# Performance work log

Hardware: AMD Instinct MI355X
Metric: run time of the kernel (lower is better)

The kernel has to match this reference:

```python
import jax, jax.numpy as jnp
import numpy as np

N_NODES = 100000
N_EDGES = 1600000
IN_DIM = 160
HID = 128
BN_EPS = 1e-5


def setup_inputs() -> dict:
    key = jax.random.key(0)
    ks = jax.random.split(key, 16)
    d = {}
    d['x'] = jax.random.normal(ks[0], (N_NODES, IN_DIM), dtype=jnp.float32)
    d['edge_index'] = jax.random.randint(ks[1], (2, N_EDGES), 0, N_NODES, dtype=jnp.int64)
    dims = [(IN_DIM, HID), (HID, HID), (HID, HID)]
    for i, (fi, fo) in enumerate(dims):
        s = 1.0 / np.sqrt(fi)
        d[f'wl{i}'] = jax.random.normal(ks[2 + 4 * i], (fi, fo), dtype=jnp.float32) * s
        d[f'wr{i}'] = jax.random.normal(ks[3 + 4 * i], (fi, fo), dtype=jnp.float32) * s
        d[f'bl{i}'] = jnp.zeros((fo,), dtype=jnp.float32)
        d[f'g{i}'] = jnp.ones((fo,), dtype=jnp.float32)
        d[f'be{i}'] = jnp.zeros((fo,), dtype=jnp.float32)
        d[f'rm{i}'] = jax.random.normal(ks[4 + 4 * i], (fo,), dtype=jnp.float32) * 0.1
        d[f'rv{i}'] = jnp.ones((fo,), dtype=jnp.float32)
    d['lin_w'] = jax.random.normal(ks[14], (HID, 1), dtype=jnp.float32) * (1.0 / np.sqrt(HID))
    d['lin_b'] = jnp.zeros((1,), dtype=jnp.float32)
    return d


def _sage_bn_relu(h, src, dst, wl, wr, bl, g, be, rm, rv):
    # mean neighbor aggregation: gather messages at src, scatter-mean to dst
    msg = h[src]                                            # [E, d]
    agg = jax.ops.segment_sum(msg, dst, num_segments=N_NODES)
    cnt = jax.ops.segment_sum(jnp.ones((msg.shape[0],), h.dtype), dst, num_segments=N_NODES)
    mean = agg / jnp.maximum(cnt, 1.0)[:, None]             # nodes w/o in-edges -> 0
    out = mean @ wl + bl + h @ wr                           # SAGEConv (root_weight=True)
    # BatchNorm1d (inference: running stats) + ReLU
    out = (out - rm) * (g * jax.lax.rsqrt(rv + BN_EPS)) + be
    return jax.nn.relu(out)


def reference(x, edge_index,
              wl0, wr0, bl0, g0, be0, rm0, rv0,
              wl1, wr1, bl1, g1, be1, rm1, rv1,
              wl2, wr2, bl2, g2, be2, rm2, rv2,
              lin_w, lin_b):
    src, dst = edge_index[0], edge_index[1]
    h = _sage_bn_relu(x, src, dst, wl0, wr0, bl0, g0, be0, rm0, rv0)
    h = _sage_bn_relu(h, src, dst, wl1, wr1, bl1, g1, be1, rm1, rv1)
    h = _sage_bn_relu(h, src, dst, wl2, wr2, bl2, g2, be2, rm2, rv2)
    return (h @ lin_w + lin_b)[:, 0]                        # [N]
```

## Files before the change

### kernel.cpp

```cpp
#include <hip/hip_runtime.h>

#define N_NODES 100000
#define N_EDGES 1600000
#define IN_DIM 160
#define HID 128
#define BN_EPS 1e-5f

#define M_PAD 100096
#define NBUCK 196
#define BSH 9
#define EPB 8192
#define NHB (NBUCK * NBUCK)
#define NSB 38
#define LPAD 132

typedef unsigned int uint;
typedef unsigned short ushort;
typedef __attribute__((ext_vector_type(8))) short bf16x8;
typedef __attribute__((ext_vector_type(4))) float f32x4;
typedef __attribute__((ext_vector_type(2))) float f32x2;

__device__ __forceinline__ ushort bf16rn(float f) {
    uint u = __float_as_uint(f);
    u += 0x7fffu + ((u >> 16) & 1u);
    return (ushort)(u >> 16);
}
__device__ __forceinline__ float bflo(uint u) { return __uint_as_float(u << 16); }
__device__ __forceinline__ float bfhi(uint u) { return __uint_as_float(u & 0xffff0000u); }


__device__ __forceinline__ void prep_body(int ob, int lane, const float* __restrict__ wl,
                                          const float* __restrict__ wr,
                                          ushort* __restrict__ Bf, int K) {
    int kb = ob >> 4;
    int tt = ob & 15;
    int n = tt * 16 + (lane & 15);
    int k0 = kb * 32 + (lane >> 4) * 8;
    ushort* dst = Bf + ((size_t)(kb * 16 + tt) * 64 + lane) * 8;
#pragma unroll
    for (int e = 0; e < 8; ++e) {
        int k = k0 + e;
        float v = (n < HID) ? wl[k * HID + n] : wr[k * HID + (n - HID)];
        dst[e] = bf16rn(v);
    }
}

#define PREP0_B 20
#define PREP1_B 16
#define INIT_GRID (NBUCK + PREP0_B + 2 * PREP1_B + 2)

__global__ __launch_bounds__(256) void init_kernel(
    const int* __restrict__ dst, int* __restrict__ ghist,
    const float* __restrict__ wl0, const float* __restrict__ wr0,
    const float* __restrict__ wl1, const float* __restrict__ wr1,
    const float* __restrict__ wl2, const float* __restrict__ wr2,
    ushort* __restrict__ Bf0, ushort* __restrict__ Bf1, ushort* __restrict__ Bf2,
    const float* __restrict__ bl0, const float* __restrict__ g0,
    const float* __restrict__ be0, const float* __restrict__ rm0,
    const float* __restrict__ rv0,
    const float* __restrict__ bl1, const float* __restrict__ g1,
    const float* __restrict__ be1, const float* __restrict__ rm1,
    const float* __restrict__ rv1,
    const float* __restrict__ bl2, const float* __restrict__ g2,
    const float* __restrict__ be2, const float* __restrict__ rm2,
    const float* __restrict__ rv2,
    float* __restrict__ bnscale, float* __restrict__ bnshift) {
    __shared__ int hist[NBUCK];
    int b = blockIdx.x, t = threadIdx.x;
    if (b < NBUCK) {
        for (int i = t; i < NBUCK; i += 256) hist[i] = 0;
        __syncthreads();
        int e0 = b * EPB;
        for (int i = 0; i < EPB; i += 256) {
            int e = e0 + i + t;
            if (e < N_EDGES) atomicAdd(&hist[dst[e] >> BSH], 1);
        }
        __syncthreads();
        for (int i = t; i < NBUCK; i += 256) ghist[i * NBUCK + b] = hist[i];
    } else if (b < NBUCK + PREP0_B) {
        int ob = (b - NBUCK) * 4 + (t >> 6);
        prep_body(ob, t & 63, wl0, wr0, Bf0, IN_DIM);
    } else if (b < NBUCK + PREP0_B + PREP1_B) {
        int ob = (b - NBUCK - PREP0_B) * 4 + (t >> 6);
        prep_body(ob, t & 63, wl1, wr1, Bf1, HID);
    } else if (b < NBUCK + PREP0_B + 2 * PREP1_B) {
        int ob = (b - NBUCK - PREP0_B - PREP1_B) * 4 + (t >> 6);
        prep_body(ob, t & 63, wl2, wr2, Bf2, HID);
    } else {
        int tt = (b - (NBUCK + PREP0_B + 2 * PREP1_B)) * 256 + t;
        if (tt < 3 * HID) {
            int L = tt >> 7, j = tt & 127;
            const float* bl = (L == 0) ? bl0 : (L == 1) ? bl1 : bl2;
            const float* gg = (L == 0) ? g0  : (L == 1) ? g1  : g2;
            const float* be = (L == 0) ? be0 : (L == 1) ? be1 : be2;
            const float* rm = (L == 0) ? rm0 : (L == 1) ? rm1 : rm2;
            const float* rv = (L == 0) ? rv0 : (L == 1) ? rv1 : rv2;
            float s = gg[j] * rsqrtf(rv[j] + BN_EPS);
            bnscale[tt] = s;
            bnshift[tt] = (bl[j] - rm[j]) * s + be[j];
        }
    }
}


__global__ __launch_bounds__(256) void scan1_kernel(const int* __restrict__ ghist,
                                                    int* __restrict__ bsum) {
    __shared__ int wsum[4];
    int b = blockIdx.x, t = threadIdx.x;
    int i4 = b * 256 + t;
    int4 v = (i4 * 4 < NHB) ? ((const int4*)ghist)[i4] : make_int4(0, 0, 0, 0);
    int s = v.x + v.y + v.z + v.w;
#pragma unroll
    for (int off = 32; off; off >>= 1) s += __shfl_down(s, off);
    if ((t & 63) == 0) wsum[t >> 6] = s;
    __syncthreads();
    if (t == 0) bsum[b] = wsum[0] + wsum[1] + wsum[2] + wsum[3];
}

__global__ void scan2_kernel(const int* __restrict__ bsum, int* __restrict__ boff,
                             int* __restrict__ gbb) {
    int lane = threadIdx.x;
    int v = (lane < NSB) ? bsum[lane] : 0;
    int s = v;
#pragma unroll
    for (int off = 1; off <= 32; off <<= 1) {
        int t2 = __shfl_up(s, off);
        if (lane >= off) s += t2;
    }
    if (lane < NSB) boff[lane] = s - v;
    if (lane == 0) gbb[NBUCK] = N_EDGES;
}

__global__ __launch_bounds__(256) void scan3_kernel(int* __restrict__ ghist,
                                                    const int* __restrict__ boff,
                                                    int* __restrict__ gbb) {
    __shared__ int ts[256];
    int b = blockIdx.x, t = threadIdx.x;
    int i4 = b * 256 + t;
    bool ok = (i4 * 4) < NHB;
    int4 v = ok ? ((const int4*)ghist)[i4] : make_int4(0, 0, 0, 0);
    int s = v.x + v.y + v.z + v.w;
    ts[t] = s;
    __syncthreads();
    for (int off = 1; off < 256; off <<= 1) {
        int a = (t >= off) ? ts[t - off] : 0;
        __syncthreads();
        ts[t] += a;
        __syncthreads();
    }
    int excl = boff[b] + ((t > 0) ? ts[t - 1] : 0);
    if (ok) {
        int idx = i4 * 4;
        int4 w;
        w.x = excl;
        w.y = excl + v.x;
        w.z = excl + v.x + v.y;
        w.w = excl + v.x + v.y + v.z;
        ((int4*)ghist)[i4] = w;
        if (idx % NBUCK == 0) gbb[idx / NBUCK] = w.x;
    }
}


__global__ __launch_bounds__(256) void bucket_csr_kernel(const uint* __restrict__ scat,
                                                         const int* __restrict__ gbb,
                                                         int* __restrict__ prow,
                                                         int* __restrict__ deg,
                                                         int* __restrict__ peidx) {
    __shared__ int cnt[512], fl[512], pref[512];
    __shared__ int ts[256];
    __shared__ int tot_s;
    int b = blockIdx.x, t = threadIdx.x;
    int beg = gbb[b], end = gbb[b + 1];
    int pb = beg + b * 8192;
    cnt[t] = 0; cnt[t + 256] = 0;
    __syncthreads();
    for (int i = beg + t; i < end; i += 256)
        atomicAdd(&cnt[scat[i] >> 17], 1);
    __syncthreads();
    int c0 = cnt[2 * t], c1 = cnt[2 * t + 1];
    int p0 = (c0 + 15) & ~15, p1 = (c1 + 15) & ~15;
    ts[t] = p0 + p1;
    __syncthreads();
    for (int off = 1; off < 256; off <<= 1) {
        int v = (t >= off) ? ts[t - off] : 0;
        __syncthreads();
        ts[t] += v;
        __syncthreads();
    }
    int ex = (t > 0) ? ts[t - 1] : 0;
    pref[2 * t] = ex;
    pref[2 * t + 1] = ex + p0;
    fl[t] = 0; fl[t + 256] = 0;
    if (t == 255) tot_s = ts[255];
    int g0 = b * 512 + 2 * t;
    if (g0 < N_NODES) { prow[g0] = pb + ex; deg[g0] = c0; }
    if (g0 + 1 < N_NODES) { prow[g0 + 1] = pb + ex + p0; deg[g0 + 1] = c1; }
    __syncthreads();
    int tot = tot_s;
    for (int i = t; i < tot; i += 256) peidx[pb + i] = N_NODES;
    __syncthreads();
    for (int i = beg + t; i < end; i += 256) {
        uint w = scat[i];
        int nl = (int)(w >> 17);
        int lp = atomicAdd(&fl[nl], 1);
        peidx[pb + pref[nl] + lp] = (int)(w & 0x1FFFFu);
    }
}

template <int K, bool AFP32>
__device__ __forceinline__ void gemm_body(int bx, int t, ushort* ldsA,
                                          const void* __restrict__ A_,
                                          const ushort* __restrict__ Bf,
                                          ushort* __restrict__ tl,
                                          ushort* __restrict__ troot) {
    constexpr int CPR = K / 8;
    constexpr int FULLG = CPR & ~7;
    const int m0b = bx * 64;

#pragma unroll
    for (int i = 0; i < (64 * CPR) / 256; ++i) {
        int cidx = i * 256 + t;
        int row = cidx / CPR;
        int j = cidx - row * CPR;
        bf16x8 v;
        if (AFP32) {
            const float* A = (const float*)A_;
            int m = m0b + row;
            float4 f0 = make_float4(0.f, 0.f, 0.f, 0.f), f1 = f0;
            if (m < N_NODES) {
                f0 = *(const float4*)(A + (size_t)m * K + j * 8);
                f1 = *(const float4*)(A + (size_t)m * K + j * 8 + 4);
            }
            v[0] = (short)bf16rn(f0.x); v[1] = (short)bf16rn(f0.y);
            v[2] = (short)bf16rn(f0.z); v[3] = (short)bf16rn(f0.w);
            v[4] = (short)bf16rn(f1.x); v[5] = (short)bf16rn(f1.y);
            v[6] = (short)bf16rn(f1.z); v[7] = (short)bf16rn(f1.w);
        } else {
            const ushort* A = (const ushort*)A_;
            v = *(const bf16x8*)(A + (size_t)(m0b + row) * K + j * 8);
        }
        int swz = (j < FULLG) ? ((j & ~7) | ((j ^ row) & 7))
                              : ((j & ~3) | ((j ^ row) & 3));
        *(bf16x8*)&ldsA[row * K + swz * 8] = v;
    }
    __syncthreads();

    const int lane = t & 63;
    const int wv = t >> 6;
    const int col = lane & 15;
    const int q = lane >> 4;
    const int rh = wv & 1;
    const int ch = wv >> 1;
    const int row0 = rh * 32 + col;
    f32x4 acc0[8], acc1[8];
#pragma unroll
    for (int tt = 0; tt < 8; ++tt) {
        acc0[tt] = (f32x4){0.f, 0.f, 0.f, 0.f};
        acc1[tt] = (f32x4){0.f, 0.f, 0.f, 0.f};
    }

#pragma unroll
    for (int kb = 0; kb < K / 32; ++kb) {
        int jj = kb * 4 + q;
        int swzj = (jj < FULLG) ? ((jj & ~7) | ((jj ^ col) & 7))
                                : ((jj & ~3) | ((jj ^ col) & 3));
        bf16x8 a0 = *(const bf16x8*)&ldsA[row0 * K + swzj * 8];
        bf16x8 a1 = *(const bf16x8*)&ldsA[(row0 + 16) * K + swzj * 8];
        const ushort* bp = Bf + ((size_t)((kb * 16 + ch * 8) * 64) + lane) * 8;
#pragma unroll
        for (int tt = 0; tt < 8; ++tt) {
            bf16x8 bfr = *(const bf16x8*)(bp + (size_t)tt * 64 * 8);
            acc0[tt] = __builtin_amdgcn_mfma_f32_16x16x32_bf16(a0, bfr, acc0[tt], 0, 0, 0);
            acc1[tt] = __builtin_amdgcn_mfma_f32_16x16x32_bf16(a1, bfr, acc1[tt], 0, 0, 0);
        }
    }

    __syncthreads();
    ushort(*rp)[16][LPAD] = (ushort(*)[16][LPAD])ldsA;
    ushort* outp = ch ? troot : tl;
#pragma unroll
    for (int mt = 0; mt < 2; ++mt) {
        const f32x4* ac = mt ? acc1 : acc0;
#pragma unroll
        for (int tt = 0; tt < 8; ++tt)
#pragma unroll
            for (int r = 0; r < 4; ++r)
                rp[wv][q * 4 + r][tt * 16 + col] = bf16rn(ac[tt][r]);
        int mbase = m0b + rh * 32 + mt * 16;
#pragma unroll
        for (int i = 0; i < 4; ++i) {
            int lin = i * 64 + lane;
            int row = lin >> 4;
            int c16 = lin & 15;
            bf16x8 v = *(const bf16x8*)&rp[wv][row][c16 * 8];
            *(bf16x8*)(outp + (size_t)(mbase + row) * HID + c16 * 8) = v;
        }
    }
}

__global__ __launch_bounds__(256) void scatter_gemm1_kernel(
    const int* __restrict__ src, const int* __restrict__ dst,
    const int* __restrict__ ghist, uint* __restrict__ scat,
    const float* __restrict__ x, const ushort* __restrict__ Bf0,
    ushort* __restrict__ tl, ushort* __restrict__ troot) {
    constexpr int LDSE = (64 * IN_DIM > 4 * 16 * LPAD) ? 64 * IN_DIM : 4 * 16 * LPAD;
    __shared__ ushort ldsA[LDSE];
    int b = blockIdx.x, t = threadIdx.x;
    if (b < NBUCK) {
        int* base = (int*)ldsA;
        int* fill = base + NBUCK;
        for (int i = t; i < NBUCK; i += 256) { base[i] = ghist[i * NBUCK + b]; fill[i] = 0; }
        __syncthreads();
        int e0 = b * EPB;
        for (int i = 0; i < EPB; i += 256) {
            int e = e0 + i + t;
            if (e < N_EDGES) {
                int d = dst[e];
                int sv = src[e];
                int bk = d >> BSH;
                int lp = atomicAdd(&fill[bk], 1);
                scat[base[bk] + lp] = (uint)sv | ((uint)(d & 511) << 17);
            }
        }
    } else {
        gemm_body<IN_DIM, true>(b - NBUCK, t, ldsA, x, Bf0, tl, troot);
    }
}

__global__ __launch_bounds__(256) void fused_agg_gemm_kernel(
    const ushort* __restrict__ tl_in, const ushort* __restrict__ troot_in,
    const int* __restrict__ prow, const int* __restrict__ deg_,
    const int* __restrict__ peidx,
    const float* __restrict__ bnscale, const float* __restrict__ bnshift,
    const ushort* __restrict__ Bf,
    ushort* __restrict__ tl_out, ushort* __restrict__ troot_out) {
    constexpr int K = HID;
    constexpr int LDSE = (64 * K > 4 * 16 * LPAD) ? 64 * K : 4 * 16 * LPAD;
    __shared__ ushort ldsA[LDSE];
    const int t = threadIdx.x;
    const int lane = t & 63;
    const int wv = t >> 6;
    const int m0b = blockIdx.x * 64;
    const int g = lane >> 4;
    const int s = lane & 15;
    const int gsel = (lane & 48) << 2;

    for (int r = 0; r < 4; ++r) {
        const int row = wv * 16 + r * 4 + g;
        const int n = m0b + row;
        const bool valid = (n < N_NODES);
        const int nn = valid ? n : 0;
        int pbeg = prow[nn];
        int dg = valid ? deg_[nn] : 0;
        int myb = (dg + 15) >> 4;

        f32x2 acc2[4];
#pragma unroll
        for (int i = 0; i < 4; ++i) acc2[i] = (f32x2){0.f, 0.f};

        bool act = (0 < myb);
        int idx = act ? peidx[pbeg + s] : N_NODES;
        int b = 0;
        while (__any(act)) {
            uint4 u[16];
#pragma unroll
            for (int jj = 0; jj < 16; ++jj) {
                int srcj = __builtin_amdgcn_ds_bpermute(gsel | (jj << 2), idx);
                u[jj] = *(const uint4*)(tl_in + (size_t)srcj * HID + s * 8);
            }
            ++b;
            bool actn = (b < myb);
            int idxn = actn ? peidx[pbeg + b * 16 + s] : N_NODES;
#pragma unroll
            for (int jj = 0; jj < 16; ++jj) {
                acc2[0] += (f32x2){bflo(u[jj].x), bfhi(u[jj].x)};
                acc2[1] += (f32x2){bflo(u[jj].y), bfhi(u[jj].y)};
                acc2[2] += (f32x2){bflo(u[jj].z), bfhi(u[jj].z)};
                acc2[3] += (f32x2){bflo(u[jj].w), bfhi(u[jj].w)};
            }
            act = actn; idx = idxn;
        }

        float inv = 1.0f / (float)((dg > 0) ? dg : 1);
        uint4 rv = *(const uint4*)(troot_in + (size_t)nn * HID + s * 8);
        float4 sc0 = *(const float4*)(bnscale + s * 8);
        float4 sc1 = *(const float4*)(bnscale + s * 8 + 4);
        float4 sh0 = *(const float4*)(bnshift + s * 8);
        float4 sh1 = *(const float4*)(bnshift + s * 8 + 4);
        float vm = valid ? 1.0f : 0.0f;
        float o[8];
        o[0] = fmaxf(fmaf(fmaf(acc2[0].x, inv, bflo(rv.x)), sc0.x, sh0.x), 0.f) * vm;
        o[1] = fmaxf(fmaf(fmaf(acc2[0].y, inv, bfhi(rv.x)), sc0.y, sh0.y), 0.f) * vm;
        o[2] = fmaxf(fmaf(fmaf(acc2[1].x, inv, bflo(rv.y)), sc0.z, sh0.z), 0.f) * vm;
        o[3] = fmaxf(fmaf(fmaf(acc2[1].y, inv, bfhi(rv.y)), sc0.w, sh0.w), 0.f) * vm;
        o[4] = fmaxf(fmaf(fmaf(acc2[2].x, inv, bflo(rv.z)), sc1.x, sh1.x), 0.f) * vm;
        o[5] = fmaxf(fmaf(fmaf(acc2[2].y, inv, bfhi(rv.z)), sc1.y, sh1.y), 0.f) * vm;
        o[6] = fmaxf(fmaf(fmaf(acc2[3].x, inv, bflo(rv.w)), sc1.z, sh1.z), 0.f) * vm;
        o[7] = fmaxf(fmaf(fmaf(acc2[3].y, inv, bfhi(rv.w)), sc1.w, sh1.w), 0.f) * vm;

        bf16x8 pk;
#pragma unroll
        for (int e = 0; e < 8; ++e) pk[e] = (short)bf16rn(o[e]);
        int swz = (s & ~7) | ((s ^ row) & 7);
        *(bf16x8*)&ldsA[row * K + swz * 8] = pk;
    }
    __syncthreads();

    const int col = lane & 15;
    const int q = lane >> 4;
    const int rh = wv & 1;
    const int ch = wv >> 1;
    const int row0 = rh * 32 + col;
    f32x4 acc0[8], acc1[8];
#pragma unroll
    for (int tt = 0; tt < 8; ++tt) {
        acc0[tt] = (f32x4){0.f, 0.f, 0.f, 0.f};
        acc1[tt] = (f32x4){0.f, 0.f, 0.f, 0.f};
    }
#pragma unroll
    for (int kb = 0; kb < K / 32; ++kb) {
        int jj = kb * 4 + q;
        int swzj = (jj & ~7) | ((jj ^ col) & 7);
        bf16x8 a0 = *(const bf16x8*)&ldsA[row0 * K + swzj * 8];
        bf16x8 a1 = *(const bf16x8*)&ldsA[(row0 + 16) * K + swzj * 8];
        const ushort* bp = Bf + ((size_t)((kb * 16 + ch * 8) * 64) + lane) * 8;
#pragma unroll
        for (int tt = 0; tt < 8; ++tt) {
            bf16x8 bfr = *(const bf16x8*)(bp + (size_t)tt * 64 * 8);
            acc0[tt] = __builtin_amdgcn_mfma_f32_16x16x32_bf16(a0, bfr, acc0[tt], 0, 0, 0);
            acc1[tt] = __builtin_amdgcn_mfma_f32_16x16x32_bf16(a1, bfr, acc1[tt], 0, 0, 0);
        }
    }

    __syncthreads();
    ushort(*rp)[16][LPAD] = (ushort(*)[16][LPAD])ldsA;
    ushort* outp = ch ? troot_out : tl_out;
#pragma unroll
    for (int mt = 0; mt < 2; ++mt) {
        const f32x4* ac = mt ? acc1 : acc0;
#pragma unroll
        for (int tt = 0; tt < 8; ++tt)
#pragma unroll
            for (int rr = 0; rr < 4; ++rr)
                rp[wv][q * 4 + rr][tt * 16 + col] = bf16rn(ac[tt][rr]);
        int mbase = m0b + rh * 32 + mt * 16;
#pragma unroll
        for (int i = 0; i < 4; ++i) {
            int lin = i * 64 + lane;
            int rowi = lin >> 4;
            int c16 = lin & 15;
            bf16x8 v = *(const bf16x8*)&rp[wv][rowi][c16 * 8];
            *(bf16x8*)(outp + (size_t)(mbase + rowi) * HID + c16 * 8) = v;
        }
    }
}

__global__ __launch_bounds__(256) void agg_final_kernel(
    const ushort* __restrict__ tl_, const ushort* __restrict__ troot_,
    const int* __restrict__ prow, const int* __restrict__ deg_,
    const int* __restrict__ peidx,
    const float* __restrict__ bnscale, const float* __restrict__ bnshift,
    const float* __restrict__ linw, const float* __restrict__ linb,
    float* __restrict__ out) {
    const int lane = threadIdx.x & 63;
    const int wvg = (blockIdx.x * 256 + (int)threadIdx.x) >> 6;
    const int g = lane >> 4;
    const int s = lane & 15;
    const int n = wvg * 4 + g;

    int pbeg = prow[n];
    int dg = deg_[n];
    int myb = (dg + 15) >> 4;

    f32x2 acc2[4];
#pragma unroll
    for (int i = 0; i < 4; ++i) acc2[i] = (f32x2){0.f, 0.f};

    const int gsel = (lane & 48) << 2;

    bool act = (0 < myb);
    int idx = act ? peidx[pbeg + s] : N_NODES;
    int b = 0;
    while (__any(act)) {
        uint4 u[16];
#pragma unroll
        for (int jj = 0; jj < 16; ++jj) {
            int srcj = __builtin_amdgcn_ds_bpermute(gsel | (jj << 2), idx);
            u[jj] = *(const uint4*)(tl_ + (size_t)srcj * HID + s * 8);
        }
        ++b;
        bool actn = (b < myb);
        int idxn = actn ? peidx[pbeg + b * 16 + s] : N_NODES;
#pragma unroll
        for (int jj = 0; jj < 16; ++jj) {
            acc2[0] += (f32x2){bflo(u[jj].x), bfhi(u[jj].x)};
            acc2[1] += (f32x2){bflo(u[jj].y), bfhi(u[jj].y)};
            acc2[2] += (f32x2){bflo(u[jj].z), bfhi(u[jj].z)};
            acc2[3] += (f32x2){bflo(u[jj].w), bfhi(u[jj].w)};
        }
        act = actn; idx = idxn;
    }

    float inv = 1.0f / (float)((dg > 0) ? dg : 1);
    uint4 rv = *(const uint4*)(troot_ + (size_t)n * HID + s * 8);
    float4 sc0 = *(const float4*)(bnscale + s * 8);
    float4 sc1 = *(const float4*)(bnscale + s * 8 + 4);
    float4 sh0 = *(const float4*)(bnshift + s * 8);
    float4 sh1 = *(const float4*)(bnshift + s * 8 + 4);
    float o[8];
    o[0] = fmaxf(fmaf(fmaf(acc2[0].x, inv, bflo(rv.x)), sc0.x, sh0.x), 0.f);
    o[1] = fmaxf(fmaf(fmaf(acc2[0].y, inv, bfhi(rv.x)), sc0.y, sh0.y), 0.f);
    o[2] = fmaxf(fmaf(fmaf(acc2[1].x, inv, bflo(rv.y)), sc0.z, sh0.z), 0.f);
    o[3] = fmaxf(fmaf(fmaf(acc2[1].y, inv, bfhi(rv.y)), sc0.w, sh0.w), 0.f);
    o[4] = fmaxf(fmaf(fmaf(acc2[2].x, inv, bflo(rv.z)), sc1.x, sh1.x), 0.f);
    o[5] = fmaxf(fmaf(fmaf(acc2[2].y, inv, bfhi(rv.z)), sc1.y, sh1.y), 0.f);
    o[6] = fmaxf(fmaf(fmaf(acc2[3].x, inv, bflo(rv.w)), sc1.z, sh1.z), 0.f);
    o[7] = fmaxf(fmaf(fmaf(acc2[3].y, inv, bfhi(rv.w)), sc1.w, sh1.w), 0.f);

    float4 w0 = *(const float4*)(linw + s * 8);
    float4 w1 = *(const float4*)(linw + s * 8 + 4);
    float p = o[0] * w0.x + o[1] * w0.y + o[2] * w0.z + o[3] * w0.w +
              o[4] * w1.x + o[5] * w1.y + o[6] * w1.z + o[7] * w1.w;
#pragma unroll
    for (int off = 1; off < 16; off <<= 1) p += __shfl_xor(p, off);
    if (s == 0) out[n] = p + linb[0];
}


extern "C" void kernel_launch(void* const* d_in, const int* in_sizes, int n_in,
                              void* d_out, int out_size, void* d_ws, size_t ws_size,
                              hipStream_t stream) {
    const float* x    = (const float*)d_in[0];
    const int*   ei   = (const int*)d_in[1];
    const int*   esrc = ei;
    const int*   edst = ei + N_EDGES;
    const float* wl[3]; const float* wr[3]; const float* bl[3];
    const float* g[3];  const float* be[3]; const float* rm[3]; const float* rv[3];
    for (int i = 0; i < 3; ++i) {
        wl[i] = (const float*)d_in[2 + 7 * i];
        wr[i] = (const float*)d_in[3 + 7 * i];
        bl[i] = (const float*)d_in[4 + 7 * i];
        g[i]  = (const float*)d_in[5 + 7 * i];
        be[i] = (const float*)d_in[6 + 7 * i];
        rm[i] = (const float*)d_in[7 + 7 * i];
        rv[i] = (const float*)d_in[8 + 7 * i];
    }
    const float* lin_w = (const float*)d_in[23];
    const float* lin_b = (const float*)d_in[24];
    float* out = (float*)d_out;

    char* ws = (char*)d_ws;
    size_t off = 0;
    auto carve = [&](size_t bytes) -> void* {
        void* p = ws + off;
        off += (bytes + 255) & ~(size_t)255;
        return p;
    };
    int*    prow   = (int*)carve((size_t)(N_NODES + 8) * sizeof(int));
    int*    deg    = (int*)carve((size_t)(N_NODES + 8) * sizeof(int));
    int*    peidx  = (int*)carve((size_t)3210000 * sizeof(int));
    uint*   scat   = (uint*)carve((size_t)N_EDGES * sizeof(uint));
    int*    ghist  = (int*)carve((size_t)(NSB * 1024) * sizeof(int));
    int*    gbb    = (int*)carve((NBUCK + 4) * sizeof(int));
    int*    bsum   = (int*)carve((NSB + 2) * sizeof(int));
    int*    boff   = (int*)carve((NSB + 2) * sizeof(int));
    ushort* tl0    = (ushort*)carve((size_t)(M_PAD + 1) * HID * sizeof(ushort));
    ushort* troot0 = (ushort*)carve((size_t)M_PAD * HID * sizeof(ushort));
    ushort* tl1    = (ushort*)carve((size_t)(M_PAD + 1) * HID * sizeof(ushort));
    ushort* troot1 = (ushort*)carve((size_t)M_PAD * HID * sizeof(ushort));
    ushort* Bf0    = (ushort*)carve(256 * IN_DIM * sizeof(ushort));
    ushort* Bf1    = (ushort*)carve(256 * HID * sizeof(ushort));
    ushort* Bf2    = (ushort*)carve(256 * HID * sizeof(ushort));
    float*  bnsc   = (float*)carve(3 * HID * sizeof(float));
    float*  bnsh   = (float*)carve(3 * HID * sizeof(float));
    (void)ws_size; (void)n_in; (void)in_sizes; (void)out_size;

    const int GEMM_GRID = M_PAD / 64;
    const int AGGF_GRID = N_NODES / 16;

    init_kernel<<<INIT_GRID, 256, 0, stream>>>(
        edst, ghist,
        wl[0], wr[0], wl[1], wr[1], wl[2], wr[2], Bf0, Bf1, Bf2,
        bl[0], g[0], be[0], rm[0], rv[0],
        bl[1], g[1], be[1], rm[1], rv[1],
        bl[2], g[2], be[2], rm[2], rv[2],
        bnsc, bnsh);
    scan1_kernel<<<NSB, 256, 0, stream>>>(ghist, bsum);
    scan2_kernel<<<1, 64, 0, stream>>>(bsum, boff, gbb);
    scan3_kernel<<<NSB, 256, 0, stream>>>(ghist, boff, gbb);
    scatter_gemm1_kernel<<<NBUCK + GEMM_GRID, 256, 0, stream>>>(
        esrc, edst, ghist, scat, x, Bf0, tl0, troot0);
    bucket_csr_kernel<<<NBUCK, 256, 0, stream>>>(scat, gbb, prow, deg, peidx);

    fused_agg_gemm_kernel<<<GEMM_GRID, 256, 0, stream>>>(
        tl0, troot0, prow, deg, peidx, bnsc, bnsh, Bf1, tl1, troot1);
    fused_agg_gemm_kernel<<<GEMM_GRID, 256, 0, stream>>>(
        tl1, troot1, prow, deg, peidx, bnsc + HID, bnsh + HID, Bf2, tl0, troot0);
    agg_final_kernel<<<AGGF_GRID, 256, 0, stream>>>(
        tl0, troot0, prow, deg, peidx, bnsc + 2 * HID, bnsh + 2 * HID,
        lin_w, lin_b, out);
}
```

Before: 435.1 us.

## Merge preprocessing kernels into one cooperative kernel with grid syncs

Replaces the init, three scan, scatter and bucket-CSR kernel launches with a single cooperative kernel that separates phases with grid-wide syncs. The layer-0 GEMM is split out into its own kernel instead of sharing a launch with the edge scatter. BN scale/shift loads are hoisted out of the per-row loop in the fused aggregation kernel. The aim is to cut launch overhead and gaps between tiny kernels, at the cost of losing the scatter/GEMM overlap and adding grid-sync latency.

Result: slower. 634.0 us (+45.7%).

```diff
diff --git a/kernel.cpp b/kernel.cpp
--- a/kernel.cpp
+++ b/kernel.cpp
@@ -1,4 +1,5 @@
 #include <hip/hip_runtime.h>
+#include <hip/hip_cooperative_groups.h>
 
 #define N_NODES 100000
 #define N_EDGES 1600000
@@ -20,6 +21,8 @@
 typedef __attribute__((ext_vector_type(4))) float f32x4;
 typedef __attribute__((ext_vector_type(2))) float f32x2;
 
+namespace cg = cooperative_groups;
+
 __device__ __forceinline__ ushort bf16rn(float f) {
     uint u = __float_as_uint(f);
     u += 0x7fffu + ((u >> 16) & 1u);
@@ -27,7 +30,6 @@
 }
 __device__ __forceinline__ float bflo(uint u) { return __uint_as_float(u << 16); }
 __device__ __forceinline__ float bfhi(uint u) { return __uint_as_float(u & 0xffff0000u); }
-
 
 __device__ __forceinline__ void prep_body(int ob, int lane, const float* __restrict__ wl,
                                           const float* __restrict__ wr,
@@ -47,164 +49,172 @@
 
 #define PREP0_B 20
 #define PREP1_B 16
-#define INIT_GRID (NBUCK + PREP0_B + 2 * PREP1_B + 2)
-
-__global__ __launch_bounds__(256) void init_kernel(
-    const int* __restrict__ dst, int* __restrict__ ghist,
-    const float* __restrict__ wl0, const float* __restrict__ wr0,
-    const float* __restrict__ wl1, const float* __restrict__ wr1,
-    const float* __restrict__ wl2, const float* __restrict__ wr2,
-    ushort* __restrict__ Bf0, ushort* __restrict__ Bf1, ushort* __restrict__ Bf2,
-    const float* __restrict__ bl0, const float* __restrict__ g0,
-    const float* __restrict__ be0, const float* __restrict__ rm0,
-    const float* __restrict__ rv0,
-    const float* __restrict__ bl1, const float* __restrict__ g1,
-    const float* __restrict__ be1, const float* __restrict__ rm1,
-    const float* __restrict__ rv1,
-    const float* __restrict__ bl2, const float* __restrict__ g2,
-    const float* __restrict__ be2, const float* __restrict__ rm2,
-    const float* __restrict__ rv2,
-    float* __restrict__ bnscale, float* __restrict__ bnshift) {
-    __shared__ int hist[NBUCK];
-    int b = blockIdx.x, t = threadIdx.x;
+#define COOP_GRID (NBUCK + PREP0_B + 2 * PREP1_B + 2)
+
+struct PreArgs {
+    const int* edst; const int* esrc;
+    int* ghist; uint* scat; int* gbb; int* bsum; int* boff;
+    int* prow; int* deg; int* peidx;
+    const float *wl0, *wr0, *wl1, *wr1, *wl2, *wr2;
+    ushort *Bf0, *Bf1, *Bf2;
+    const float *bl0, *g0, *be0, *rm0, *rv0;
+    const float *bl1, *g1, *be1, *rm1, *rv1;
+    const float *bl2, *g2, *be2, *rm2, *rv2;
+    float *bnsc, *bnsh;
+};
+
+__global__ __launch_bounds__(256) void coop_pre_kernel(PreArgs a) {
+    cg::grid_group grid = cg::this_grid();
+    __shared__ union {
+        int hist[NBUCK];
+        struct { int wsum[4]; } s1;
+        struct { int ts[256]; } s3;
+        struct { int base[NBUCK]; int fill[NBUCK]; } sc;
+        struct { int cnt[512]; int fl[512]; int pref[512]; int ts[256]; int tot; } csr;
+    } u;
+    const int b = blockIdx.x, t = threadIdx.x;
+
     if (b < NBUCK) {
-        for (int i = t; i < NBUCK; i += 256) hist[i] = 0;
+        for (int i = t; i < NBUCK; i += 256) u.hist[i] = 0;
         __syncthreads();
         int e0 = b * EPB;
         for (int i = 0; i < EPB; i += 256) {
             int e = e0 + i + t;
-            if (e < N_EDGES) atomicAdd(&hist[dst[e] >> BSH], 1);
-        }
-        __syncthreads();
-        for (int i = t; i < NBUCK; i += 256) ghist[i * NBUCK + b] = hist[i];
+            if (e < N_EDGES) atomicAdd(&u.hist[a.edst[e] >> BSH], 1);
+        }
+        __syncthreads();
+        for (int i = t; i < NBUCK; i += 256) a.ghist[i * NBUCK + b] = u.hist[i];
     } else if (b < NBUCK + PREP0_B) {
-        int ob = (b - NBUCK) * 4 + (t >> 6);
-        prep_body(ob, t & 63, wl0, wr0, Bf0, IN_DIM);
+        prep_body((b - NBUCK) * 4 + (t >> 6), t & 63, a.wl0, a.wr0, a.Bf0, IN_DIM);
     } else if (b < NBUCK + PREP0_B + PREP1_B) {
-        int ob = (b - NBUCK - PREP0_B) * 4 + (t >> 6);
-        prep_body(ob, t & 63, wl1, wr1, Bf1, HID);
+        prep_body((b - NBUCK - PREP0_B) * 4 + (t >> 6), t & 63, a.wl1, a.wr1, a.Bf1, HID);
     } else if (b < NBUCK + PREP0_B + 2 * PREP1_B) {
-        int ob = (b - NBUCK - PREP0_B - PREP1_B) * 4 + (t >> 6);
-        prep_body(ob, t & 63, wl2, wr2, Bf2, HID);
+        prep_body((b - NBUCK - PREP0_B - PREP1_B) * 4 + (t >> 6), t & 63, a.wl2, a.wr2, a.Bf2, HID);
     } else {
         int tt = (b - (NBUCK + PREP0_B + 2 * PREP1_B)) * 256 + t;
         if (tt < 3 * HID) {
             int L = tt >> 7, j = tt & 127;
-            const float* bl = (L == 0) ? bl0 : (L == 1) ? bl1 : bl2;
-            const float* gg = (L == 0) ? g0  : (L == 1) ? g1  : g2;
-            const float* be = (L == 0) ? be0 : (L == 1) ? be1 : be2;
-            const float* rm = (L == 0) ? rm0 : (L == 1) ? rm1 : rm2;
-            const float* rv = (L == 0) ? rv0 : (L == 1) ? rv1 : rv2;
+            const float* bl = (L == 0) ? a.bl0 : (L == 1) ? a.bl1 : a.bl2;
+            const float* gg = (L == 0) ? a.g0  : (L == 1) ? a.g1  : a.g2;
+            const float* be = (L == 0) ? a.be0 : (L == 1) ? a.be1 : a.be2;
+            const float* rm = (L == 0) ? a.rm0 : (L == 1) ? a.rm1 : a.rm2;
+            const float* rv = (L == 0) ? a.rv0 : (L == 1) ? a.rv1 : a.rv2;
             float s = gg[j] * rsqrtf(rv[j] + BN_EPS);
-            bnscale[tt] = s;
-            bnshift[tt] = (bl[j] - rm[j]) * s + be[j];
-        }
-    }
-}
-
-
-__global__ __launch_bounds__(256) void scan1_kernel(const int* __restrict__ ghist,
-                                                    int* __restrict__ bsum) {
-    __shared__ int wsum[4];
-    int b = blockIdx.x, t = threadIdx.x;
-    int i4 = b * 256 + t;
-    int4 v = (i4 * 4 < NHB) ? ((const int4*)ghist)[i4] : make_int4(0, 0, 0, 0);
-    int s = v.x + v.y + v.z + v.w;
-#pragma unroll
-    for (int off = 32; off; off >>= 1) s += __shfl_down(s, off);
-    if ((t & 63) == 0) wsum[t >> 6] = s;
-    __syncthreads();
-    if (t == 0) bsum[b] = wsum[0] + wsum[1] + wsum[2] + wsum[3];
-}
-
-__global__ void scan2_kernel(const int* __restrict__ bsum, int* __restrict__ boff,
-                             int* __restrict__ gbb) {
-    int lane = threadIdx.x;
-    int v = (lane < NSB) ? bsum[lane] : 0;
-    int s = v;
-#pragma unroll
-    for (int off = 1; off <= 32; off <<= 1) {
-        int t2 = __shfl_up(s, off);
-        if (lane >= off) s += t2;
-    }
-    if (lane < NSB) boff[lane] = s - v;
-    if (lane == 0) gbb[NBUCK] = N_EDGES;
-}
-
-__global__ __launch_bounds__(256) void scan3_kernel(int* __restrict__ ghist,
-                                                    const int* __restrict__ boff,
-                                                    int* __restrict__ gbb) {
-    __shared__ int ts[256];
-    int b = blockIdx.x, t = threadIdx.x;
-    int i4 = b * 256 + t;
-    bool ok = (i4 * 4) < NHB;
-    int4 v = ok ? ((const int4*)ghist)[i4] : make_int4(0, 0, 0, 0);
-    int s = v.x + v.y + v.z + v.w;
-    ts[t] = s;
-    __syncthreads();
-    for (int off = 1; off < 256; off <<= 1) {
-        int a = (t >= off) ? ts[t - off] : 0;
-        __syncthreads();
-        ts[t] += a;
-        __syncthreads();
-    }
-    int excl = boff[b] + ((t > 0) ? ts[t - 1] : 0);
-    if (ok) {
-        int idx = i4 * 4;
-        int4 w;
-        w.x = excl;
-        w.y = excl + v.x;
-        w.z = excl + v.x + v.y;
-        w.w = excl + v.x + v.y + v.z;
-        ((int4*)ghist)[i4] = w;
-        if (idx % NBUCK == 0) gbb[idx / NBUCK] = w.x;
-    }
-}
-
-
-__global__ __launch_bounds__(256) void bucket_csr_kernel(const uint* __restrict__ scat,
-                                                         const int* __restrict__ gbb,
-                                                         int* __restrict__ prow,
-                                                         int* __restrict__ deg,
-                                                         int* __restrict__ peidx) {
-    __shared__ int cnt[512], fl[512], pref[512];
-    __shared__ int ts[256];
-    __shared__ int tot_s;
-    int b = blockIdx.x, t = threadIdx.x;
-    int beg = gbb[b], end = gbb[b + 1];
-    int pb = beg + b * 8192;
-    cnt[t] = 0; cnt[t + 256] = 0;
-    __syncthreads();
-    for (int i = beg + t; i < end; i += 256)
-        atomicAdd(&cnt[scat[i] >> 17], 1);
-    __syncthreads();
-    int c0 = cnt[2 * t], c1 = cnt[2 * t + 1];
-    int p0 = (c0 + 15) & ~15, p1 = (c1 + 15) & ~15;
-    ts[t] = p0 + p1;
-    __syncthreads();
-    for (int off = 1; off < 256; off <<= 1) {
-        int v = (t >= off) ? ts[t - off] : 0;
-        __syncthreads();
-        ts[t] += v;
-        __syncthreads();
-    }
-    int ex = (t > 0) ? ts[t - 1] : 0;
-    pref[2 * t] = ex;
-    pref[2 * t + 1] = ex + p0;
-    fl[t] = 0; fl[t + 256] = 0;
-    if (t == 255) tot_s = ts[255];
-    int g0 = b * 512 + 2 * t;
-    if (g0 < N_NODES) { prow[g0] = pb + ex; deg[g0] = c0; }
-    if (g0 + 1 < N_NODES) { prow[g0 + 1] = pb + ex + p0; deg[g0 + 1] = c1; }
-    __syncthreads();
-    int tot = tot_s;
-    for (int i = t; i < tot; i += 256) peidx[pb + i] = N_NODES;
-    __syncthreads();
-    for (int i = beg + t; i < end; i += 256) {
-        uint w = scat[i];
-        int nl = (int)(w >> 17);
-        int lp = atomicAdd(&fl[nl], 1);
-        peidx[pb + pref[nl] + lp] = (int)(w & 0x1FFFFu);
+            a.bnsc[tt] = s;
+            a.bnsh[tt] = (bl[j] - rm[j]) * s + be[j];
+        }
+    }
+    grid.sync();
+
+    if (b < NSB) {
+        int i4 = b * 256 + t;
+        int4 v = (i4 * 4 < NHB) ? ((const int4*)a.ghist)[i4] : make_int4(0, 0, 0, 0);
+        int s = v.x + v.y + v.z + v.w;
+#pragma unroll
+        for (int off = 32; off; off >>= 1) s += __shfl_down(s, off);
+        if ((t & 63) == 0) u.s1.wsum[t >> 6] = s;
+        __syncthreads();
+        if (t == 0) a.bsum[b] = u.s1.wsum[0] + u.s1.wsum[1] + u.s1.wsum[2] + u.s1.wsum[3];
+    }
+    grid.sync();
+
+    if (b == 0 && t < 64) {
+        int lane = t;
+        int v = (lane < NSB) ? a.bsum[lane] : 0;
+        int s = v;
+#pragma unroll
+        for (int off = 1; off <= 32; off <<= 1) {
+            int t2 = __shfl_up(s, off);
+            if (lane >= off) s += t2;
+        }
+        if (lane < NSB) a.boff[lane] = s - v;
+        if (lane == 0) a.gbb[NBUCK] = N_EDGES;
+    }
+    grid.sync();
+
+    if (b < NSB) {
+        int i4 = b * 256 + t;
+        bool ok = (i4 * 4) < NHB;
+        int4 v = ok ? ((const int4*)a.ghist)[i4] : make_int4(0, 0, 0, 0);
+        int s = v.x + v.y + v.z + v.w;
+        u.s3.ts[t] = s;
+        __syncthreads();
+        for (int off = 1; off < 256; off <<= 1) {
+            int x2 = (t >= off) ? u.s3.ts[t - off] : 0;
+            __syncthreads();
+            u.s3.ts[t] += x2;
+            __syncthreads();
+        }
+        int excl = a.boff[b] + ((t > 0) ? u.s3.ts[t - 1] : 0);
+        if (ok) {
+            int idx = i4 * 4;
+            int4 w;
+            w.x = excl;
+            w.y = excl + v.x;
+            w.z = excl + v.x + v.y;
+            w.w = excl + v.x + v.y + v.z;
+            ((int4*)a.ghist)[i4] = w;
+            if (idx % NBUCK == 0) a.gbb[idx / NBUCK] = w.x;
+        }
+    }
+    grid.sync();
+
+    if (b < NBUCK) {
+        for (int i = t; i < NBUCK; i += 256) {
+            u.sc.base[i] = a.ghist[i * NBUCK + b];
+            u.sc.fill[i] = 0;
+        }
+        __syncthreads();
+        int e0 = b * EPB;
+        for (int i = 0; i < EPB; i += 256) {
+            int e = e0 + i + t;
+            if (e < N_EDGES) {
+                int d = a.edst[e];
+                int sv = a.esrc[e];
+                int bk = d >> BSH;
+                int lp = atomicAdd(&u.sc.fill[bk], 1);
+                a.scat[u.sc.base[bk] + lp] = (uint)sv | ((uint)(d & 511) << 17);
+            }
+        }
+    }
+    grid.sync();
+
+    if (b < NBUCK) {
+        int beg = a.gbb[b], end = a.gbb[b + 1];
+        int pb = beg + b * 8192;
+        u.csr.cnt[t] = 0; u.csr.cnt[t + 256] = 0;
+        __syncthreads();
+        for (int i = beg + t; i < end; i += 256)
+            atomicAdd(&u.csr.cnt[a.scat[i] >> 17], 1);
+        __syncthreads();
+        int c0 = u.csr.cnt[2 * t], c1 = u.csr.cnt[2 * t + 1];
+        int p0 = (c0 + 15) & ~15, p1 = (c1 + 15) & ~15;
+        u.csr.ts[t] = p0 + p1;
+        __syncthreads();
+        for (int off = 1; off < 256; off <<= 1) {
+            int v = (t >= off) ? u.csr.ts[t - off] : 0;
+            __syncthreads();
+            u.csr.ts[t] += v;
+            __syncthreads();
+        }
+        int ex = (t > 0) ? u.csr.ts[t - 1] : 0;
+        u.csr.pref[2 * t] = ex;
+        u.csr.pref[2 * t + 1] = ex + p0;
+        u.csr.fl[t] = 0; u.csr.fl[t + 256] = 0;
+        if (t == 255) u.csr.tot = u.csr.ts[255];
+        int g0 = b * 512 + 2 * t;
+        if (g0 < N_NODES) { a.prow[g0] = pb + ex; a.deg[g0] = c0; }
+        if (g0 + 1 < N_NODES) { a.prow[g0 + 1] = pb + ex + p0; a.deg[g0 + 1] = c1; }
+        __syncthreads();
+        int tot = u.csr.tot;
+        for (int i = t; i < tot; i += 256) a.peidx[pb + i] = N_NODES;
+        __syncthreads();
+        for (int i = beg + t; i < end; i += 256) {
+            uint w = a.scat[i];
+            int nl = (int)(w >> 17);
+            int lp = atomicAdd(&u.csr.fl[nl], 1);
+            a.peidx[pb + u.csr.pref[nl] + lp] = (int)(w & 0x1FFFFu);
+        }
     }
 }
 
@@ -299,33 +309,14 @@
     }
 }
 
-__global__ __launch_bounds__(256) void scatter_gemm1_kernel(
-    const int* __restrict__ src, const int* __restrict__ dst,
-    const int* __restrict__ ghist, uint* __restrict__ scat,
-    const float* __restrict__ x, const ushort* __restrict__ Bf0,
-    ushort* __restrict__ tl, ushort* __restrict__ troot) {
-    constexpr int LDSE = (64 * IN_DIM > 4 * 16 * LPAD) ? 64 * IN_DIM : 4 * 16 * LPAD;
+template <int K, bool AFP32>
+__global__ __launch_bounds__(256) void gemm_kernel(const void* __restrict__ A_,
+                                                   const ushort* __restrict__ Bf,
+                                                   ushort* __restrict__ tl,
+                                                   ushort* __restrict__ troot) {
+    constexpr int LDSE = (64 * K > 4 * 16 * LPAD) ? 64 * K : 4 * 16 * LPAD;
     __shared__ ushort ldsA[LDSE];
-    int b = blockIdx.x, t = threadIdx.x;
-    if (b < NBUCK) {
-        int* base = (int*)ldsA;
-        int* fill = base + NBUCK;
-        for (int i = t; i < NBUCK; i += 256) { base[i] = ghist[i * NBUCK + b]; fill[i] = 0; }
-        __syncthreads();
-        int e0 = b * EPB;
-        for (int i = 0; i < EPB; i += 256) {
-            int e = e0 + i + t;
-            if (e < N_EDGES) {
-                int d = dst[e];
-                int sv = src[e];
-                int bk = d >> BSH;
-                int lp = atomicAdd(&fill[bk], 1);
-                scat[base[bk] + lp] = (uint)sv | ((uint)(d & 511) << 17);
-            }
-        }
-    } else {
-        gemm_body<IN_DIM, true>(b - NBUCK, t, ldsA, x, Bf0, tl, troot);
-    }
+    gemm_body<K, AFP32>(blockIdx.x, threadIdx.x, ldsA, A_, Bf, tl, troot);
 }
 
 __global__ __launch_bounds__(256) void fused_agg_gemm_kernel(
@@ -346,6 +337,11 @@
     const int s = lane & 15;
     const int gsel = (lane & 48) << 2;
 
+    float4 sc0 = *(const float4*)(bnscale + s * 8);
+    float4 sc1 = *(const float4*)(bnscale + s * 8 + 4);
+    float4 sh0 = *(const float4*)(bnshift + s * 8);
+    float4 sh1 = *(const float4*)(bnshift + s * 8 + 4);
+
     for (int r = 0; r < 4; ++r) {
         const int row = wv * 16 + r * 4 + g;
         const int n = m0b + row;
@@ -384,10 +380,6 @@
 
         float inv = 1.0f / (float)((dg > 0) ? dg : 1);
         uint4 rv = *(const uint4*)(troot_in + (size_t)nn * HID + s * 8);
-        float4 sc0 = *(const float4*)(bnscale + s * 8);
-        float4 sc1 = *(const float4*)(bnscale + s * 8 + 4);
-        float4 sh0 = *(const float4*)(bnshift + s * 8);
-        float4 sh1 = *(const float4*)(bnshift + s * 8 + 4);
         float vm = valid ? 1.0f : 0.0f;
         float o[8];
         o[0] = fmaxf(fmaf(fmaf(acc2[0].x, inv, bflo(rv.x)), sc0.x, sh0.x), 0.f) * vm;
@@ -579,19 +571,22 @@
     const int GEMM_GRID = M_PAD / 64;
     const int AGGF_GRID = N_NODES / 16;
 
-    init_kernel<<<INIT_GRID, 256, 0, stream>>>(
-        edst, ghist,
-        wl[0], wr[0], wl[1], wr[1], wl[2], wr[2], Bf0, Bf1, Bf2,
-        bl[0], g[0], be[0], rm[0], rv[0],
-        bl[1], g[1], be[1], rm[1], rv[1],
-        bl[2], g[2], be[2], rm[2], rv[2],
-        bnsc, bnsh);
-    scan1_kernel<<<NSB, 256, 0, stream>>>(ghist, bsum);
-    scan2_kernel<<<1, 64, 0, stream>>>(bsum, boff, gbb);
-    scan3_kernel<<<NSB, 256, 0, stream>>>(ghist, boff, gbb);
-    scatter_gemm1_kernel<<<NBUCK + GEMM_GRID, 256, 0, stream>>>(
-        esrc, edst, ghist, scat, x, Bf0, tl0, troot0);
-    bucket_csr_kernel<<<NBUCK, 256, 0, stream>>>(scat, gbb, prow, deg, peidx);
+    PreArgs pa;
+    pa.edst = edst; pa.esrc = esrc;
+    pa.ghist = ghist; pa.scat = scat; pa.gbb = gbb; pa.bsum = bsum; pa.boff = boff;
+    pa.prow = prow; pa.deg = deg; pa.peidx = peidx;
+    pa.wl0 = wl[0]; pa.wr0 = wr[0]; pa.wl1 = wl[1]; pa.wr1 = wr[1];
+    pa.wl2 = wl[2]; pa.wr2 = wr[2];
+    pa.Bf0 = Bf0; pa.Bf1 = Bf1; pa.Bf2 = Bf2;
+    pa.bl0 = bl[0]; pa.g0 = g[0]; pa.be0 = be[0]; pa.rm0 = rm[0]; pa.rv0 = rv[0];
+    pa.bl1 = bl[1]; pa.g1 = g[1]; pa.be1 = be[1]; pa.rm1 = rm[1]; pa.rv1 = rv[1];
+    pa.bl2 = bl[2]; pa.g2 = g[2]; pa.be2 = be[2]; pa.rm2 = rm[2]; pa.rv2 = rv[2];
+    pa.bnsc = bnsc; pa.bnsh = bnsh;
+    void* kargs[] = { &pa };
+    hipLaunchCooperativeKernel((const void*)coop_pre_kernel, dim3(COOP_GRID), dim3(256),
+                               kargs, 0, stream);
+
+    gemm_kernel<IN_DIM, true><<<GEMM_GRID, 256, 0, stream>>>(x, Bf0, tl0, troot0);
 
     fused_agg_gemm_kernel<<<GEMM_GRID, 256, 0, stream>>>(
         tl0, troot0, prow, deg, peidx, bnsc, bnsh, Bf1, tl1, troot1);
```
